# Performance work log

Measured on AMD Instinct MI355X. Metric: run time of the kernel, lower is better.

Reference implementation:

```python
import jax, jax.numpy as jnp
import numpy as np

MIN_SCORE = 0.3       # min_score_threshold
NMS_THRESHOLD = 0.3   # nms_threshold
MAX_OUT = 256         # fixed output padding (jit-compatible replacement for dynamic K)


def _cxcywh_to_xyxy(b):
    cx, cy, w, h = b[..., 0], b[..., 1], b[..., 2], b[..., 3]
    half_w, half_h = w * 0.5, h * 0.5
    return jnp.stack([cx - half_w, cy - half_h, cx + half_w, cy + half_h], axis=-1)


def _pairwise_iou(a, b):
    # a: [N,4], b: [M,4] in xyxy
    lt = jnp.maximum(a[:, None, :2], b[None, :, :2])
    rb = jnp.minimum(a[:, None, 2:], b[None, :, 2:])
    wh = jnp.clip(rb - lt, 0.0)
    inter = wh[..., 0] * wh[..., 1]
    area_a = (a[:, 2] - a[:, 0]) * (a[:, 3] - a[:, 1])
    area_b = (b[:, 2] - b[:, 0]) * (b[:, 3] - b[:, 1])
    return inter / (area_a[:, None] + area_b[None, :] - inter + 1e-9)


def setup_inputs() -> dict:
    key = jax.random.key(0)
    k1, k2 = jax.random.split(key)
    N, n_coords = 8192, 16
    score = jax.random.uniform(k1, (N, 1), dtype=jnp.float32)
    box = jax.random.uniform(k2, (N, n_coords), dtype=jnp.float32)
    return {"score": score, "box": box}


def reference(score, box):
    # score: [N,1], box: [N,n_coords]; single class (n_classes==1, cls=None)
    s = score[:, 0]
    valid = s >= MIN_SCORE                      # score mask applied before NMS
    order = jnp.argsort(-s)                     # score-descending (batched_nms order)
    s_s = s[order]
    v_s = valid[order]
    box_s = box[order]
    bbox = _cxcywh_to_xyxy(box_s[:, :4]).astype(jnp.float32)
    iou = _pairwise_iou(bbox, bbox)             # [N,N]
    N = s.shape[0]

    def body(kept, i):
        # suppressed if overlaps any already-kept (higher-score) box
        suppressed = jnp.any(kept & (iou[:, i] > NMS_THRESHOLD))
        keep_i = v_s[i] & jnp.logical_not(suppressed)
        return kept.at[i].set(keep_i), None

    kept, _ = jax.lax.scan(body, jnp.zeros((N,), dtype=bool), jnp.arange(N))

    # compact kept detections to the front, preserving score order (stable sort)
    comp = jnp.argsort(jnp.where(kept, 0, 1), stable=True)[:MAX_OUT]
    out_valid = kept[comp]                      # [MAX_OUT]
    score_out = jnp.where(out_valid[:, None], s_s[comp][:, None], 0.0)   # [MAX_OUT,1]
    box_out = jnp.where(out_valid[:, None], box_s[comp], 0.0)            # [MAX_OUT,n_coords]
    return score_out, box_out, out_valid
```

## Files before the change

### kernel.cpp

```cpp
#include <hip/hip_runtime.h>
#include <stdint.h>

typedef unsigned long long u64;

#define N 8192
#define NW 128
#define MAX_OUT 256
#define MASK_BYTES ((size_t)N * NW * 8)


__global__ __launch_bounds__(1024)
void rank_fused_kernel(const float* __restrict__ score, const float* __restrict__ box,
                       int* __restrict__ order, float* __restrict__ s_s,
                       float4* __restrict__ bbox, float* __restrict__ area,
                       int* __restrict__ nvalid) {
    __shared__ uint32_t ksc[N];
    __shared__ int psum[32][33];
    __shared__ int vpart[16];
    const int tid = threadIdx.x;

    const float4* s4 = (const float4*)score;
    float4 a = s4[tid * 2], b = s4[tid * 2 + 1];
    ksc[tid * 8 + 0] = __float_as_uint(a.x);
    ksc[tid * 8 + 1] = __float_as_uint(a.y);
    ksc[tid * 8 + 2] = __float_as_uint(a.z);
    ksc[tid * 8 + 3] = __float_as_uint(a.w);
    ksc[tid * 8 + 4] = __float_as_uint(b.x);
    ksc[tid * 8 + 5] = __float_as_uint(b.y);
    ksc[tid * 8 + 6] = __float_as_uint(b.z);
    ksc[tid * 8 + 7] = __float_as_uint(b.w);
    int c = (a.x >= 0.3f) + (a.y >= 0.3f) + (a.z >= 0.3f) + (a.w >= 0.3f)
          + (b.x >= 0.3f) + (b.y >= 0.3f) + (b.z >= 0.3f) + (b.w >= 0.3f);
    for (int off = 32; off; off >>= 1) c += __shfl_down(c, off);
    if ((tid & 63) == 0) vpart[tid >> 6] = c;
    __syncthreads();
    if (blockIdx.x == 0 && tid == 0) {
        int t = 0;
        #pragma unroll
        for (int w = 0; w < 16; ++w) t += vpart[w];
        *nvalid = t;
    }

    const int i_local = tid & 31;
    const int jg = tid >> 5;
    const int ibase = blockIdx.x * 32;
    const uint32_t si = ksc[ibase + i_local];
    const int i = ibase + i_local;
    int cnt = 0;
    const int j0 = jg * 256;
    #pragma unroll 8
    for (int t = 0; t < 256; ++t) {
        const int j = j0 + t;
        const uint32_t sj = ksc[j];
        cnt += (sj > si || (sj == si && j < i)) ? 1 : 0;
    }
    psum[i_local][jg] = cnt;
    __syncthreads();

    if (tid < 32) {
        int r = 0;
        #pragma unroll
        for (int k = 0; k < 32; ++k) r += psum[tid][k];
        const int ii = ibase + tid;
        order[r] = ii;
        s_s[r] = score[ii];
        float4 cb = ((const float4*)box)[ii * 4];
        float hw = cb.z * 0.5f, hh = cb.w * 0.5f;
        float x0 = cb.x - hw, y0 = cb.y - hh, x1 = cb.x + hw, y1 = cb.y + hh;
        bbox[r] = make_float4(x0, y0, x1, y1);
        area[r] = (x1 - x0) * (y1 - y0);
    }
}

__global__ __launch_bounds__(256)
void mask_kernel(const float4* __restrict__ bbox, const float* __restrict__ area,
                 const int* __restrict__ nvalid_p, u64* __restrict__ maskT) {
    const int w = blockIdx.x;
    if (w < (int)(blockIdx.y << 2)) return;
    const int nv = *nvalid_p;
    if ((int)(blockIdx.y * 256) >= nv) return;
    __shared__ float4 jb[64];
    __shared__ float  ja[64];
    if (threadIdx.x < 64) {
        jb[threadIdx.x] = bbox[w * 64 + threadIdx.x];
        ja[threadIdx.x] = area[w * 64 + threadIdx.x];
    }
    __syncthreads();
    const int i = blockIdx.y * 256 + threadIdx.x;
    if (i >= nv) return;
    if (w < (i >> 6)) return;
    float4 aa4 = bbox[i];
    float  aa = area[i];
    u64 bits = 0, fb = 0;
    #pragma unroll 8
    for (int jj = 0; jj < 64; ++jj) {
        float4 b = jb[jj];
        float lx = fmaxf(aa4.x, b.x), ly = fmaxf(aa4.y, b.y);
        float rx = fminf(aa4.z, b.z), ry = fminf(aa4.w, b.w);
        float ww = fmaxf(rx - lx, 0.0f), hh = fmaxf(ry - ly, 0.0f);
        float inter = ww * hh;
        float denom = ((aa + ja[jj]) - inter) + 1e-9f;
        float d = fmaf(-0.3f, denom, inter);
        bits |= ((u64)(d > 0.0f)) << jj;
        fb   |= ((u64)(fabsf(d) <= 1e-5f * denom)) << jj;
    }
    if (fb) {
        while (fb) {
            int jj = (int)__builtin_ctzll(fb); fb &= fb - 1;
            float4 b = jb[jj];
            float lx = fmaxf(aa4.x, b.x), ly = fmaxf(aa4.y, b.y);
            float rx = fminf(aa4.z, b.z), ry = fminf(aa4.w, b.w);
            float ww = fmaxf(rx - lx, 0.0f), hh = fmaxf(ry - ly, 0.0f);
            float inter = ww * hh;
            float denom = ((aa + ja[jj]) - inter) + 1e-9f;
            float iou = inter / denom;
            bits = (bits & ~(1ull << jj)) | (((u64)(iou > 0.3f)) << jj);
        }
    }
    maskT[(size_t)w * N + i] = bits;
}

struct Pipe { u64 col, s1, s2, g0, g1, g2, g3; };

__device__ __forceinline__ unsigned or_dpp32(unsigned v) {
    v |= (unsigned)__builtin_amdgcn_update_dpp(0, (int)v, 0x111, 0xf, 0xf, true);
    v |= (unsigned)__builtin_amdgcn_update_dpp(0, (int)v, 0x112, 0xf, 0xf, true);
    v |= (unsigned)__builtin_amdgcn_update_dpp(0, (int)v, 0x114, 0xf, 0xf, true);
    v |= (unsigned)__builtin_amdgcn_update_dpp(0, (int)v, 0x118, 0xf, 0xf, true);
    v |= (unsigned)__builtin_amdgcn_update_dpp(0, (int)v, 0x142, 0xf, 0xf, true);
    v |= (unsigned)__builtin_amdgcn_update_dpp(0, (int)v, 0x143, 0xf, 0xf, true);
    return v;
}

__device__ __forceinline__ u64 wave_or64(u64 v) {
    unsigned lo = or_dpp32((unsigned)v);
    unsigned hi = or_dpp32((unsigned)(v >> 32));
    unsigned slo = (unsigned)__builtin_amdgcn_readlane((int)lo, 63);
    unsigned shi = (unsigned)__builtin_amdgcn_readlane((int)hi, 63);
    return ((u64)shi << 32) | (u64)slo;
}

__global__ __launch_bounds__(64)
void nms_kernel(const u64* __restrict__ maskT, const float* __restrict__ s_s,
                const int* __restrict__ order, const float* __restrict__ box,
                const int* __restrict__ nvalid_p, float* __restrict__ out) {
    const int lane = threadIdx.x;
    const int nv = *nvalid_p;
    const int nblk = (nv + 63) >> 6;
    int kcount = 0;
    int kp0 = 0, kp1 = 0, kp2 = 0, kp3 = 0;
    u64 s1m = 0, s2m = 0, s2m_old = 0;

    Pipe A, B;
    A.col = A.s1 = A.s2 = A.g0 = A.g1 = A.g2 = A.g3 = 0;
    B.col = B.s1 = B.s2 = B.g0 = B.g1 = B.g2 = B.g3 = 0;
    if (nblk > 0) {
        A.col = maskT[lane];
        if (nblk > 1) A.s1 = maskT[(size_t)1 * N + lane];
        if (nblk > 2) A.s2 = maskT[(size_t)2 * N + lane];
    }
    if (nblk > 1) {
        B.col = maskT[(size_t)1 * N + 64 + lane];
        if (nblk > 2) B.s1 = maskT[(size_t)2 * N + 64 + lane];
        if (nblk > 3) B.s2 = maskT[(size_t)3 * N + 64 + lane];
    }

    auto step = [&](int b, Pipe& P) -> bool {
        u64 col = P.col, s1v = P.s1, s2v = P.s2;
        u64 x = P.g0 | P.g1 | P.g2 | P.g3 | s1m | s2m_old;
        const int b2 = b + 2;
        P.col = P.s1 = P.s2 = P.g0 = P.g1 = P.g2 = P.g3 = 0;
        if (b2 < nblk) {
            const int row = (b2 << 6) + lane;
            P.col = maskT[(size_t)b2 * N + row];
            if (b2 + 1 < nblk) P.s1 = maskT[(size_t)(b2 + 1) * N + row];
            if (b2 + 2 < nblk) P.s2 = maskT[(size_t)(b2 + 2) * N + row];
            const int kc = kcount;
            const u64* colw = maskT + (size_t)b2 * N;
            if (lane < kc)       P.g0 = colw[kp0];
            if (lane +  64 < kc) P.g1 = colw[kp1];
            if (lane + 128 < kc) P.g2 = colw[kp2];
            if (lane + 192 < kc) P.g3 = colw[kp3];
        }
        u64 rw = wave_or64(x);
        const int base = b << 6;
        const int rem = nv - base;
        u64 validm = (rem >= 64) ? ~0ull : ((1ull << rem) - 1ull);
        u64 todo = validm & ~rw;
        u64 km = 0;
        while (todo) {
            int l = (int)__builtin_ctzll(todo);
            u64 row_l = __ballot(((col >> l) & 1ull) != 0);
            const int pos = base + l;
            const bool own = (lane == (kcount & 63));
            const int slot = kcount >> 6;
            kp0 = (own && slot == 0) ? pos : kp0;
            kp1 = (own && slot == 1) ? pos : kp1;
            kp2 = (own && slot == 2) ? pos : kp2;
            kp3 = (own && slot == 3) ? pos : kp3;
            km |= (1ull << l);
            kcount++;
            todo &= ~(row_l | (1ull << l));
            if (kcount >= MAX_OUT) break;
        }
        u64 keepm = ((km >> lane) & 1ull) ? ~0ull : 0ull;
        s2m_old = s2m;
        s2m = s2v & keepm;
        s1m = s1v & keepm;
        return kcount < MAX_OUT;
    };

    bool run = true;
    for (int b = 0; run && b < nblk; b += 2) {
        run = step(b, A);
        if (run && b + 1 < nblk) run = step(b + 1, B);
    }

    float* out_score = out;
    float* out_box   = out + MAX_OUT;
    float* out_valid = out + MAX_OUT + MAX_OUT * 16;
    const float4* box4 = (const float4*)box;
    float4* ob4 = (float4*)out_box;
    #define EMIT_SLOT(Q, KP) do {                                              \
        const int t = lane + 64 * (Q);                                         \
        if (t < kcount) {                                                      \
            int p = (KP);                                                      \
            out_score[t] = s_s[p];                                             \
            out_valid[t] = 1.0f;                                               \
            int oi = order[p];                                                 \
            _Pragma("unroll")                                                  \
            for (int q = 0; q < 4; ++q) ob4[t * 4 + q] = box4[oi * 4 + q];     \
        } else {                                                               \
            out_score[t] = 0.0f;                                               \
            out_valid[t] = 0.0f;                                               \
            float4 z = make_float4(0.f, 0.f, 0.f, 0.f);                        \
            _Pragma("unroll")                                                  \
            for (int q = 0; q < 4; ++q) ob4[t * 4 + q] = z;                    \
        }                                                                      \
    } while (0)
    EMIT_SLOT(0, kp0);
    EMIT_SLOT(1, kp1);
    EMIT_SLOT(2, kp2);
    EMIT_SLOT(3, kp3);
    #undef EMIT_SLOT
}

extern "C" void kernel_launch(void* const* d_in, const int* in_sizes, int n_in,
                              void* d_out, int out_size, void* d_ws, size_t ws_size,
                              hipStream_t stream) {
    const float* score = (const float*)d_in[0];
    const float* box   = (const float*)d_in[1];
    char* ws = (char*)d_ws;
    u64*    maskT  = (u64*)ws;
    int*    order  = (int*)   (ws + MASK_BYTES);
    float*  s_s    = (float*) (ws + MASK_BYTES + 32768);
    float4* bbox   = (float4*)(ws + MASK_BYTES + 65536);
    float*  area   = (float*) (ws + MASK_BYTES + 65536 + 131072);
    int*    nvalid = (int*)   (ws + MASK_BYTES + 65536 + 131072 + 32768);

    rank_fused_kernel<<<256, 1024, 0, stream>>>(score, box, order, s_s, bbox, area, nvalid);
    mask_kernel<<<dim3(128, 32), 256, 0, stream>>>(bbox, area, nvalid, maskT);
    nms_kernel<<<1, 64, 0, stream>>>(maskT, s_s, order, box, nvalid, (float*)d_out);
}
```

Baseline: 128.1 us.

## Process NMS in 128-box superblocks with in-loop cross-block suppression

Restructures the serial NMS scan to handle two 64-box blocks per iteration. Suppression of the second block by boxes kept in the first is folded in during the first block's loop via readlane ORs, and carries from both blocks are merged for the next two word columns. This halves the number of wave-wide OR reductions and loop iterations on the serial critical path. The cost is an extra pair of readlanes per kept box, more registers, and more prefetch loads per iteration.

```diff
diff --git a/kernel.cpp b/kernel.cpp
--- a/kernel.cpp
+++ b/kernel.cpp
@@ -120,7 +120,6 @@
     maskT[(size_t)w * N + i] = bits;
 }
 
-struct Pipe { u64 col, s1, s2, g0, g1, g2, g3; };
 
 __device__ __forceinline__ unsigned or_dpp32(unsigned v) {
     v |= (unsigned)__builtin_amdgcn_update_dpp(0, (int)v, 0x111, 0xf, 0xf, true);
@@ -140,6 +139,9 @@
     return ((u64)shi << 32) | (u64)slo;
 }
 
+#define RL64(v, l) ( ((u64)(unsigned)__builtin_amdgcn_readlane((int)(unsigned)((v) >> 32), (l)) << 32) \
+                   |  (u64)(unsigned)__builtin_amdgcn_readlane((int)(unsigned)(v), (l)) )
+
 __global__ __launch_bounds__(64)
 void nms_kernel(const u64* __restrict__ maskT, const float* __restrict__ s_s,
                 const int* __restrict__ order, const float* __restrict__ box,
@@ -147,50 +149,87 @@
     const int lane = threadIdx.x;
     const int nv = *nvalid_p;
     const int nblk = (nv + 63) >> 6;
+    const int nst = (nblk + 1) >> 1;
     int kcount = 0;
     int kp0 = 0, kp1 = 0, kp2 = 0, kp3 = 0;
-    u64 s1m = 0, s2m = 0, s2m_old = 0;
-
-    Pipe A, B;
-    A.col = A.s1 = A.s2 = A.g0 = A.g1 = A.g2 = A.g3 = 0;
-    B.col = B.s1 = B.s2 = B.g0 = B.g1 = B.g2 = B.g3 = 0;
-    if (nblk > 0) {
-        A.col = maskT[lane];
-        if (nblk > 1) A.s1 = maskT[(size_t)1 * N + lane];
-        if (nblk > 2) A.s2 = maskT[(size_t)2 * N + lane];
-    }
-    if (nblk > 1) {
-        B.col = maskT[(size_t)1 * N + 64 + lane];
-        if (nblk > 2) B.s1 = maskT[(size_t)2 * N + 64 + lane];
-        if (nblk > 3) B.s2 = maskT[(size_t)3 * N + 64 + lane];
-    }
-
-    auto step = [&](int b, Pipe& P) -> bool {
-        u64 col = P.col, s1v = P.s1, s2v = P.s2;
-        u64 x = P.g0 | P.g1 | P.g2 | P.g3 | s1m | s2m_old;
-        const int b2 = b + 2;
-        P.col = P.s1 = P.s2 = P.g0 = P.g1 = P.g2 = P.g3 = 0;
-        if (b2 < nblk) {
-            const int row = (b2 << 6) + lane;
-            P.col = maskT[(size_t)b2 * N + row];
-            if (b2 + 1 < nblk) P.s1 = maskT[(size_t)(b2 + 1) * N + row];
-            if (b2 + 2 < nblk) P.s2 = maskT[(size_t)(b2 + 2) * N + row];
+    u64 carry0 = 0, carry1 = 0;
+
+    u64 pc00 = 0, pc10 = 0, pc11 = 0;
+    u64 ps00 = 0, ps01 = 0, ps10 = 0, ps11 = 0;
+    u64 pg0=0, pg1=0, pg2=0, pg3=0, ph0=0, ph1=0, ph2=0, ph3=0;
+
+    if (nst > 0) {
+        pc00 = maskT[lane];
+        if (1 < nblk) {
+            pc10 = maskT[(size_t)1 * N + lane];
+            pc11 = maskT[(size_t)1 * N + 64 + lane];
+        }
+        if (2 < nblk) {
+            ps00 = maskT[(size_t)2 * N + lane];
+            ps01 = maskT[(size_t)2 * N + 64 + lane];
+        }
+        if (3 < nblk) {
+            ps10 = maskT[(size_t)3 * N + lane];
+            ps11 = maskT[(size_t)3 * N + 64 + lane];
+        }
+    }
+
+    for (int t = 0; t < nst && kcount < MAX_OUT; ++t) {
+        u64 c00 = pc00, c10 = pc10, c11 = pc11;
+        u64 x0 = pg0 | pg1 | pg2 | pg3 | carry0;
+        u64 x1 = ph0 | ph1 | ph2 | ph3 | carry1;
+        u64 s00 = ps00, s01 = ps01, s10 = ps10, s11 = ps11;
+
+        pc00 = pc10 = pc11 = 0;
+        ps00 = ps01 = ps10 = ps11 = 0;
+        pg0 = pg1 = pg2 = pg3 = ph0 = ph1 = ph2 = ph3 = 0;
+        const int t1 = t + 1;
+        if (t1 < nst) {
+            const int w0n = t1 << 1, w1n = w0n | 1;
+            const size_t r0n = ((size_t)t1 << 7) + lane;
+            const u64* cw0 = maskT + (size_t)w0n * N;
             const int kc = kcount;
-            const u64* colw = maskT + (size_t)b2 * N;
-            if (lane < kc)       P.g0 = colw[kp0];
-            if (lane +  64 < kc) P.g1 = colw[kp1];
-            if (lane + 128 < kc) P.g2 = colw[kp2];
-            if (lane + 192 < kc) P.g3 = colw[kp3];
-        }
-        u64 rw = wave_or64(x);
-        const int base = b << 6;
-        const int rem = nv - base;
-        u64 validm = (rem >= 64) ? ~0ull : ((1ull << rem) - 1ull);
-        u64 todo = validm & ~rw;
-        u64 km = 0;
+            pc00 = cw0[r0n];
+            if (lane < kc)        pg0 = cw0[kp0];
+            if (lane +  64 < kc)  pg1 = cw0[kp1];
+            if (lane + 128 < kc)  pg2 = cw0[kp2];
+            if (lane + 192 < kc)  pg3 = cw0[kp3];
+            if (w1n < nblk) {
+                const u64* cw1 = maskT + (size_t)w1n * N;
+                pc10 = cw1[r0n];
+                pc11 = cw1[r0n + 64];
+                if (lane < kc)        ph0 = cw1[kp0];
+                if (lane +  64 < kc)  ph1 = cw1[kp1];
+                if (lane + 128 < kc)  ph2 = cw1[kp2];
+                if (lane + 192 < kc)  ph3 = cw1[kp3];
+            }
+            const int ws0 = w0n + 2, ws1 = w0n + 3;
+            if (ws0 < nblk) {
+                const u64* sw0 = maskT + (size_t)ws0 * N;
+                ps00 = sw0[r0n];
+                ps01 = sw0[r0n + 64];
+            }
+            if (ws1 < nblk) {
+                const u64* sw1 = maskT + (size_t)ws1 * N;
+                ps10 = sw1[r0n];
+                ps11 = sw1[r0n + 64];
+            }
+        }
+
+        u64 rw0 = wave_or64(x0);
+        u64 rw1 = wave_or64(x1);
+
+        const int base = t << 7;
+        const int rem0 = nv - base;
+        const int rem1 = rem0 - 64;
+        u64 vm0 = (rem0 >= 64) ? ~0ull : ((1ull << rem0) - 1ull);
+        u64 vm1 = (rem1 >= 64) ? ~0ull : ((rem1 > 0) ? ((1ull << rem1) - 1ull) : 0ull);
+
+        u64 km0 = 0, km1 = 0;
+        u64 todo = vm0 & ~rw0;
         while (todo) {
             int l = (int)__builtin_ctzll(todo);
-            u64 row_l = __ballot(((col >> l) & 1ull) != 0);
+            u64 row_l = __ballot(((c00 >> l) & 1ull) != 0);
             const int pos = base + l;
             const bool own = (lane == (kcount & 63));
             const int slot = kcount >> 6;
@@ -198,22 +237,34 @@
             kp1 = (own && slot == 1) ? pos : kp1;
             kp2 = (own && slot == 2) ? pos : kp2;
             kp3 = (own && slot == 3) ? pos : kp3;
-            km |= (1ull << l);
+            km0 |= 1ull << l;
             kcount++;
             todo &= ~(row_l | (1ull << l));
+            rw1 |= RL64(c10, l);
             if (kcount >= MAX_OUT) break;
         }
-        u64 keepm = ((km >> lane) & 1ull) ? ~0ull : 0ull;
-        s2m_old = s2m;
-        s2m = s2v & keepm;
-        s1m = s1v & keepm;
-        return kcount < MAX_OUT;
-    };
-
-    bool run = true;
-    for (int b = 0; run && b < nblk; b += 2) {
-        run = step(b, A);
-        if (run && b + 1 < nblk) run = step(b + 1, B);
+        if (kcount < MAX_OUT) {
+            todo = vm1 & ~rw1;
+            while (todo) {
+                int l = (int)__builtin_ctzll(todo);
+                u64 row_l = __ballot(((c11 >> l) & 1ull) != 0);
+                const int pos = base + 64 + l;
+                const bool own = (lane == (kcount & 63));
+                const int slot = kcount >> 6;
+                kp0 = (own && slot == 0) ? pos : kp0;
+                kp1 = (own && slot == 1) ? pos : kp1;
+                kp2 = (own && slot == 2) ? pos : kp2;
+                kp3 = (own && slot == 3) ? pos : kp3;
+                km1 |= 1ull << l;
+                kcount++;
+                todo &= ~(row_l | (1ull << l));
+                if (kcount >= MAX_OUT) break;
+            }
+        }
+        u64 keepm0 = ((km0 >> lane) & 1ull) ? ~0ull : 0ull;
+        u64 keepm1 = ((km1 >> lane) & 1ull) ? ~0ull : 0ull;
+        carry0 = (s00 & keepm0) | (s01 & keepm1);
+        carry1 = (s10 & keepm0) | (s11 & keepm1);
     }
 
     float* out_score = out;
```

New measurement: 129.9 us. No clear change (+1.4%).

## Process NMS blocks in 128-row super-steps with dual-word prefetch pipeline

Applied to the files above, without the earlier changes.

Restructures the serial NMS sweep so each pipeline stage handles two 64-bit mask words (128 boxes) at once. The kept-list gather loads, carries and prefetches are issued for both words together, and suppression from the first half feeds the second half via readlane. The aim is to halve the number of serial stage transitions and wave-wide OR reductions, so more memory latency hides behind the dependent ballot loop. The cost is many more live 64-bit registers and extra prefetched loads, some of which may be wasted after early termination.

```diff
diff --git a/kernel.cpp b/kernel.cpp
--- a/kernel.cpp
+++ b/kernel.cpp
@@ -120,7 +120,6 @@
     maskT[(size_t)w * N + i] = bits;
 }
 
-struct Pipe { u64 col, s1, s2, g0, g1, g2, g3; };
 
 __device__ __forceinline__ unsigned or_dpp32(unsigned v) {
     v |= (unsigned)__builtin_amdgcn_update_dpp(0, (int)v, 0x111, 0xf, 0xf, true);
@@ -140,80 +139,151 @@
     return ((u64)shi << 32) | (u64)slo;
 }
 
-__global__ __launch_bounds__(64)
+#define RL64(v, l) ( ((u64)(unsigned)__builtin_amdgcn_readlane((int)(unsigned)((v) >> 32), (l)) << 32) \
+                   |  (u64)(unsigned)__builtin_amdgcn_readlane((int)(unsigned)(v), (l)) )
+
+#define NMS_STEP(T, PC00,PC10,PC11, S1A0,S1A1,S1B0,S1B1, S2A0,S2A1,S2B0,S2B1,  \
+                 G0,G1,G2,G3, H0,H1,H2,H3) do {                                \
+    const int t_ = (T);                                                        \
+                   \
+    u64 c00_ = PC00, c10_ = PC10, c11_ = PC11;                                 \
+    u64 x0_ = G0 | G1 | G2 | G3 | carry1_0 | carry2_0;                         \
+    u64 x1_ = H0 | H1 | H2 | H3 | carry1_1 | carry2_1;                         \
+    u64 s1a0_=S1A0, s1a1_=S1A1, s1b0_=S1B0, s1b1_=S1B1;                        \
+    u64 s2a0_=S2A0, s2a1_=S2A1, s2b0_=S2B0, s2b1_=S2B1;                        \
+         \
+    PC00=0; PC10=0; PC11=0;                                                    \
+    S1A0=0; S1A1=0; S1B0=0; S1B1=0; S2A0=0; S2A1=0; S2B0=0; S2B1=0;            \
+    G0=0; G1=0; G2=0; G3=0; H0=0; H1=0; H2=0; H3=0;                            \
+    const int t2_ = t_ + 2;                                                    \
+    if (t2_ < nst) {                                                           \
+        const int w0n_ = t2_ << 1, w1n_ = w0n_ | 1;                            \
+        const size_t r0_ = ((size_t)t2_ << 7) + lane;                          \
+        const u64* cw0_ = maskT + (size_t)w0n_ * N;                            \
+        const int kc_ = kcount;                                                \
+        PC00 = cw0_[r0_];                                                      \
+        if (lane < kc_)        G0 = cw0_[kp0];                                 \
+        if (lane +  64 < kc_)  G1 = cw0_[kp1];                                 \
+        if (lane + 128 < kc_)  G2 = cw0_[kp2];                                 \
+        if (lane + 192 < kc_)  G3 = cw0_[kp3];                                 \
+        if (w1n_ < nblk) {                                                     \
+            const u64* cw1_ = maskT + (size_t)w1n_ * N;                        \
+            PC10 = cw1_[r0_];                                                  \
+            PC11 = cw1_[r0_ + 64];                                             \
+            if (lane < kc_)        H0 = cw1_[kp0];                             \
+            if (lane +  64 < kc_)  H1 = cw1_[kp1];                             \
+            if (lane + 128 < kc_)  H2 = cw1_[kp2];                             \
+            if (lane + 192 < kc_)  H3 = cw1_[kp3];                             \
+        }                                                                      \
+        if (w0n_ + 2 < nblk) { const u64* p_ = maskT + (size_t)(w0n_+2)*N;     \
+                               S1A0 = p_[r0_]; S1A1 = p_[r0_ + 64]; }          \
+        if (w0n_ + 3 < nblk) { const u64* p_ = maskT + (size_t)(w0n_+3)*N;     \
+                               S1B0 = p_[r0_]; S1B1 = p_[r0_ + 64]; }          \
+        if (w0n_ + 4 < nblk) { const u64* p_ = maskT + (size_t)(w0n_+4)*N;     \
+                               S2A0 = p_[r0_]; S2A1 = p_[r0_ + 64]; }          \
+        if (w0n_ + 5 < nblk) { const u64* p_ = maskT + (size_t)(w0n_+5)*N;     \
+                               S2B0 = p_[r0_]; S2B1 = p_[r0_ + 64]; }          \
+    }                                                                          \
+                           \
+    u64 rw0_ = wave_or64(x0_);                                                 \
+    u64 rw1_ = wave_or64(x1_);                                                 \
+    const int base_ = t_ << 7;                                                 \
+    const int rem0_ = nv - base_;                                              \
+    const int rem1_ = rem0_ - 64;                                              \
+    u64 vm0_ = (rem0_ >= 64) ? ~0ull : ((1ull << rem0_) - 1ull);               \
+    u64 vm1_ = (rem1_ >= 64) ? ~0ull : ((rem1_ > 0) ? ((1ull << rem1_) - 1ull) : 0ull); \
+    u64 km0_ = 0, km1_ = 0;                                                    \
+    u64 todo_ = vm0_ & ~rw0_;                                                  \
+    while (todo_) {                                                            \
+        int l_ = (int)__builtin_ctzll(todo_);                                  \
+        u64 rowl_ = __ballot(((c00_ >> l_) & 1ull) != 0);                      \
+        const int pos_ = base_ + l_;                                           \
+        const bool own_ = (lane == (kcount & 63));                             \
+        const int slot_ = kcount >> 6;                                         \
+        kp0 = (own_ && slot_ == 0) ? pos_ : kp0;                               \
+        kp1 = (own_ && slot_ == 1) ? pos_ : kp1;                               \
+        kp2 = (own_ && slot_ == 2) ? pos_ : kp2;                               \
+        kp3 = (own_ && slot_ == 3) ? pos_ : kp3;                               \
+        km0_ |= 1ull << l_;                                                    \
+        kcount++;                                                              \
+        todo_ &= ~(rowl_ | (1ull << l_));                                      \
+        rw1_ |= RL64(c10_, l_);                                                \
+        if (kcount >= MAX_OUT) break;                                          \
+    }                                                                          \
+    if (kcount < MAX_OUT) {                                                    \
+        todo_ = vm1_ & ~rw1_;                                                  \
+        while (todo_) {                                                        \
+            int l_ = (int)__builtin_ctzll(todo_);                              \
+            u64 rowl_ = __ballot(((c11_ >> l_) & 1ull) != 0);                  \
+            const int pos_ = base_ + 64 + l_;                                  \
+            const bool own_ = (lane == (kcount & 63));                         \
+            const int slot_ = kcount >> 6;                                     \
+            kp0 = (own_ && slot_ == 0) ? pos_ : kp0;                           \
+            kp1 = (own_ && slot_ == 1) ? pos_ : kp1;                           \
+            kp2 = (own_ && slot_ == 2) ? pos_ : kp2;                           \
+            kp3 = (own_ && slot_ == 3) ? pos_ : kp3;                           \
+            km1_ |= 1ull << l_;                                                \
+            kcount++;                                                          \
+            todo_ &= ~(rowl_ | (1ull << l_));                                  \
+            if (kcount >= MAX_OUT) break;                                      \
+        }                                                                      \
+    }                                                                          \
+          \
+    u64 keepm0_ = ((km0_ >> lane) & 1ull) ? ~0ull : 0ull;                      \
+    u64 keepm1_ = ((km1_ >> lane) & 1ull) ? ~0ull : 0ull;                      \
+    carry1_0 = (s1a0_ & keepm0_) | (s1a1_ & keepm1_);                          \
+    carry1_1 = (s1b0_ & keepm0_) | (s1b1_ & keepm1_);                          \
+    carry2_0 = c2pend0; carry2_1 = c2pend1;                                    \
+    c2pend0 = (s2a0_ & keepm0_) | (s2a1_ & keepm1_);                           \
+    c2pend1 = (s2b0_ & keepm0_) | (s2b1_ & keepm1_);                           \
+} while (0)
+
+__global__ __launch_bounds__(64, 1)
 void nms_kernel(const u64* __restrict__ maskT, const float* __restrict__ s_s,
                 const int* __restrict__ order, const float* __restrict__ box,
                 const int* __restrict__ nvalid_p, float* __restrict__ out) {
     const int lane = threadIdx.x;
     const int nv = *nvalid_p;
     const int nblk = (nv + 63) >> 6;
+    const int nst = (nblk + 1) >> 1;
     int kcount = 0;
     int kp0 = 0, kp1 = 0, kp2 = 0, kp3 = 0;
-    u64 s1m = 0, s2m = 0, s2m_old = 0;
-
-    Pipe A, B;
-    A.col = A.s1 = A.s2 = A.g0 = A.g1 = A.g2 = A.g3 = 0;
-    B.col = B.s1 = B.s2 = B.g0 = B.g1 = B.g2 = B.g3 = 0;
-    if (nblk > 0) {
-        A.col = maskT[lane];
-        if (nblk > 1) A.s1 = maskT[(size_t)1 * N + lane];
-        if (nblk > 2) A.s2 = maskT[(size_t)2 * N + lane];
-    }
-    if (nblk > 1) {
-        B.col = maskT[(size_t)1 * N + 64 + lane];
-        if (nblk > 2) B.s1 = maskT[(size_t)2 * N + 64 + lane];
-        if (nblk > 3) B.s2 = maskT[(size_t)3 * N + 64 + lane];
-    }
-
-    auto step = [&](int b, Pipe& P) -> bool {
-        u64 col = P.col, s1v = P.s1, s2v = P.s2;
-        u64 x = P.g0 | P.g1 | P.g2 | P.g3 | s1m | s2m_old;
-        const int b2 = b + 2;
-        P.col = P.s1 = P.s2 = P.g0 = P.g1 = P.g2 = P.g3 = 0;
-        if (b2 < nblk) {
-            const int row = (b2 << 6) + lane;
-            P.col = maskT[(size_t)b2 * N + row];
-            if (b2 + 1 < nblk) P.s1 = maskT[(size_t)(b2 + 1) * N + row];
-            if (b2 + 2 < nblk) P.s2 = maskT[(size_t)(b2 + 2) * N + row];
-            const int kc = kcount;
-            const u64* colw = maskT + (size_t)b2 * N;
-            if (lane < kc)       P.g0 = colw[kp0];
-            if (lane +  64 < kc) P.g1 = colw[kp1];
-            if (lane + 128 < kc) P.g2 = colw[kp2];
-            if (lane + 192 < kc) P.g3 = colw[kp3];
-        }
-        u64 rw = wave_or64(x);
-        const int base = b << 6;
-        const int rem = nv - base;
-        u64 validm = (rem >= 64) ? ~0ull : ((1ull << rem) - 1ull);
-        u64 todo = validm & ~rw;
-        u64 km = 0;
-        while (todo) {
-            int l = (int)__builtin_ctzll(todo);
-            u64 row_l = __ballot(((col >> l) & 1ull) != 0);
-            const int pos = base + l;
-            const bool own = (lane == (kcount & 63));
-            const int slot = kcount >> 6;
-            kp0 = (own && slot == 0) ? pos : kp0;
-            kp1 = (own && slot == 1) ? pos : kp1;
-            kp2 = (own && slot == 2) ? pos : kp2;
-            kp3 = (own && slot == 3) ? pos : kp3;
-            km |= (1ull << l);
-            kcount++;
-            todo &= ~(row_l | (1ull << l));
-            if (kcount >= MAX_OUT) break;
-        }
-        u64 keepm = ((km >> lane) & 1ull) ? ~0ull : 0ull;
-        s2m_old = s2m;
-        s2m = s2v & keepm;
-        s1m = s1v & keepm;
-        return kcount < MAX_OUT;
-    };
-
-    bool run = true;
-    for (int b = 0; run && b < nblk; b += 2) {
-        run = step(b, A);
-        if (run && b + 1 < nblk) run = step(b + 1, B);
+    u64 carry1_0 = 0, carry1_1 = 0;
+    u64 carry2_0 = 0, carry2_1 = 0;
+    u64 c2pend0 = 0, c2pend1 = 0;
+
+    u64 apc00=0, apc10=0, apc11=0;
+    u64 as1a0=0, as1a1=0, as1b0=0, as1b1=0, as2a0=0, as2a1=0, as2b0=0, as2b1=0;
+    u64 ag0=0, ag1=0, ag2=0, ag3=0, ah0=0, ah1=0, ah2=0, ah3=0;
+    u64 bpc00=0, bpc10=0, bpc11=0;
+    u64 bs1a0=0, bs1a1=0, bs1b0=0, bs1b1=0, bs2a0=0, bs2a1=0, bs2b0=0, bs2b1=0;
+    u64 bg0=0, bg1=0, bg2=0, bg3=0, bh0=0, bh1=0, bh2=0, bh3=0;
+
+    if (nst > 0) {
+        const size_t r0 = (size_t)lane;
+        apc00 = maskT[r0];
+        if (1 < nblk) { apc10 = maskT[(size_t)1*N + r0]; apc11 = maskT[(size_t)1*N + r0 + 64]; }
+        if (2 < nblk) { as1a0 = maskT[(size_t)2*N + r0]; as1a1 = maskT[(size_t)2*N + r0 + 64]; }
+        if (3 < nblk) { as1b0 = maskT[(size_t)3*N + r0]; as1b1 = maskT[(size_t)3*N + r0 + 64]; }
+        if (4 < nblk) { as2a0 = maskT[(size_t)4*N + r0]; as2a1 = maskT[(size_t)4*N + r0 + 64]; }
+        if (5 < nblk) { as2b0 = maskT[(size_t)5*N + r0]; as2b1 = maskT[(size_t)5*N + r0 + 64]; }
+    }
+    if (1 < nst) {
+        const size_t r1 = (size_t)128 + lane;
+        bpc00 = maskT[(size_t)2*N + r1];
+        if (3 < nblk) { bpc10 = maskT[(size_t)3*N + r1]; bpc11 = maskT[(size_t)3*N + r1 + 64]; }
+        if (4 < nblk) { bs1a0 = maskT[(size_t)4*N + r1]; bs1a1 = maskT[(size_t)4*N + r1 + 64]; }
+        if (5 < nblk) { bs1b0 = maskT[(size_t)5*N + r1]; bs1b1 = maskT[(size_t)5*N + r1 + 64]; }
+        if (6 < nblk) { bs2a0 = maskT[(size_t)6*N + r1]; bs2a1 = maskT[(size_t)6*N + r1 + 64]; }
+        if (7 < nblk) { bs2b0 = maskT[(size_t)7*N + r1]; bs2b1 = maskT[(size_t)7*N + r1 + 64]; }
+    }
+
+    for (int t = 0; t < nst && kcount < MAX_OUT; t += 2) {
+        NMS_STEP(t, apc00,apc10,apc11, as1a0,as1a1,as1b0,as1b1,
+                 as2a0,as2a1,as2b0,as2b1, ag0,ag1,ag2,ag3, ah0,ah1,ah2,ah3);
+        if (t + 1 < nst && kcount < MAX_OUT)
+            NMS_STEP(t + 1, bpc00,bpc10,bpc11, bs1a0,bs1a1,bs1b0,bs1b1,
+                     bs2a0,bs2a1,bs2b0,bs2b1, bg0,bg1,bg2,bg3, bh0,bh1,bh2,bh3);
     }
 
     float* out_score = out;
```

Result: slower. 131.1 us (+2.3%).

## Track removal bitmask per lane via row loads instead of gathered columns

Applied to the files above, without the earlier changes.

Replaces the per-block gather of kept boxes' column words plus a wave-wide DPP OR reduction with a running per-lane removal vector (two u64 words covering 128 blocks). Each lane accumulates the mask rows of newly kept boxes, and the block's suppression word is read with readlane. Immediate next-block suppression is handled by readlane of the s1 row for each kept box, and the first four kept rows are prefetched and deferred one step. This aims to shorten the serial dependency chain per block, at the cost of strided per-lane loads and extra readlane loops proportional to kept boxes.

```diff
diff --git a/kernel.cpp b/kernel.cpp
--- a/kernel.cpp
+++ b/kernel.cpp
@@ -120,27 +120,84 @@
     maskT[(size_t)w * N + i] = bits;
 }
 
-struct Pipe { u64 col, s1, s2, g0, g1, g2, g3; };
-
-__device__ __forceinline__ unsigned or_dpp32(unsigned v) {
-    v |= (unsigned)__builtin_amdgcn_update_dpp(0, (int)v, 0x111, 0xf, 0xf, true);
-    v |= (unsigned)__builtin_amdgcn_update_dpp(0, (int)v, 0x112, 0xf, 0xf, true);
-    v |= (unsigned)__builtin_amdgcn_update_dpp(0, (int)v, 0x114, 0xf, 0xf, true);
-    v |= (unsigned)__builtin_amdgcn_update_dpp(0, (int)v, 0x118, 0xf, 0xf, true);
-    v |= (unsigned)__builtin_amdgcn_update_dpp(0, (int)v, 0x142, 0xf, 0xf, true);
-    v |= (unsigned)__builtin_amdgcn_update_dpp(0, (int)v, 0x143, 0xf, 0xf, true);
-    return v;
-}
-
-__device__ __forceinline__ u64 wave_or64(u64 v) {
-    unsigned lo = or_dpp32((unsigned)v);
-    unsigned hi = or_dpp32((unsigned)(v >> 32));
-    unsigned slo = (unsigned)__builtin_amdgcn_readlane((int)lo, 63);
-    unsigned shi = (unsigned)__builtin_amdgcn_readlane((int)hi, 63);
-    return ((u64)shi << 32) | (u64)slo;
-}
-
-__global__ __launch_bounds__(64)
+
+#define RL64(v, l) ( ((u64)(unsigned)__builtin_amdgcn_readlane((int)(unsigned)((v) >> 32), (l)) << 32) \
+                   |  (u64)(unsigned)__builtin_amdgcn_readlane((int)(unsigned)(v), (l)) )
+
+#define NMS_STEP(B, PCOL, PS1, D0,D1,D2,D3,D4,D5,D6,D7, DCNT) do {            \
+    const int b_ = (B);                                                        \
+      \
+    {                                                                          \
+        const int c_ = DCNT;                                                   \
+        remv0 |= (c_ > 0 ? D0 : 0) | (c_ > 1 ? D2 : 0)                         \
+               | (c_ > 2 ? D4 : 0) | (c_ > 3 ? D6 : 0);                        \
+        remv1 |= (c_ > 0 ? D1 : 0) | (c_ > 1 ? D3 : 0)                         \
+               | (c_ > 2 ? D5 : 0) | (c_ > 3 ? D7 : 0);                        \
+    }                                                                          \
+                                  \
+    u64 sel_ = (b_ < 64) ? remv0 : remv1;                                      \
+    u64 rw_ = RL64(sel_, b_ & 63) | rsup;                                      \
+                 \
+    u64 col_ = PCOL;                                                           \
+    u64 s1v_ = (b_ + 1 < nblk) ? PS1 : 0;                                      \
+           \
+    {                                                                          \
+        const int nb1_ = nblk - 1;                                             \
+        const int bc_ = (b_ + 2 < nb1_) ? (b_ + 2) : nb1_;                     \
+        const int w1_ = (b_ + 3 < nb1_) ? (b_ + 3) : nb1_;                     \
+        const int row_ = (bc_ << 6) + lane;                                    \
+        PCOL = maskT[(size_t)bc_ * N + row_];                                  \
+        PS1  = maskT[(size_t)w1_ * N + row_];                                  \
+    }                                                                          \
+                                                               \
+    const int base_ = b_ << 6;                                                 \
+    const int rem_ = nv - base_;                                               \
+    u64 validm_ = (rem_ >= 64) ? ~0ull : ((1ull << rem_) - 1ull);              \
+    u64 todo_ = validm_ & ~rw_;                                                \
+    u64 km_ = 0;                                                               \
+    while (todo_) {                                                            \
+        int l_ = (int)__builtin_ctzll(todo_);                                  \
+        u64 rowl_ = __ballot(((col_ >> l_) & 1ull) != 0);                      \
+        const int pos_ = base_ + l_;                                           \
+        const bool own_ = (lane == (kcount & 63));                             \
+        const int slot_ = kcount >> 6;                                         \
+        kp0 = (own_ && slot_ == 0) ? pos_ : kp0;                               \
+        kp1 = (own_ && slot_ == 1) ? pos_ : kp1;                               \
+        kp2 = (own_ && slot_ == 2) ? pos_ : kp2;                               \
+        kp3 = (own_ && slot_ == 3) ? pos_ : kp3;                               \
+        km_ |= (1ull << l_);                                                   \
+        kcount++;                                                              \
+           \
+        todo_ &= ~(rowl_ | (1ull << l_));                                      \
+        if (kcount >= MAX_OUT) break;                                          \
+    }                                                                          \
+    \
+    u64 add1_ = 0, t_ = km_;                                                   \
+    while (t_) { int l_ = (int)__builtin_ctzll(t_); t_ &= t_ - 1;              \
+                 add1_ |= RL64(s1v_, l_); }                                    \
+    rsup = add1_;                                                              \
+        \
+    {                                                                          \
+        u64 t2_ = km_;                                                         \
+        int r0_ = base_, r1_ = base_, r2_ = base_, r3_ = base_, c2_ = 0;       \
+        if (t2_) { r0_ = base_ + (int)__builtin_ctzll(t2_); t2_ &= t2_ - 1; c2_ = 1; } \
+        if (t2_) { r1_ = base_ + (int)__builtin_ctzll(t2_); t2_ &= t2_ - 1; c2_ = 2; } \
+        if (t2_) { r2_ = base_ + (int)__builtin_ctzll(t2_); t2_ &= t2_ - 1; c2_ = 3; } \
+        if (t2_) { r3_ = base_ + (int)__builtin_ctzll(t2_); t2_ &= t2_ - 1; c2_ = 4; } \
+        D0 = maskT[woffL + r0_]; D1 = maskT[woffH + r0_];                      \
+        D2 = maskT[woffL + r1_]; D3 = maskT[woffH + r1_];                      \
+        D4 = maskT[woffL + r2_]; D5 = maskT[woffH + r2_];                      \
+        D6 = maskT[woffL + r3_]; D7 = maskT[woffH + r3_];                      \
+        DCNT = c2_;                                                            \
+                \
+        while (t2_) { int l_ = (int)__builtin_ctzll(t2_); t2_ &= t2_ - 1;      \
+                      const int r_ = base_ + l_;                               \
+                      remv0 |= maskT[woffL + r_]; remv1 |= maskT[woffH + r_]; }\
+    }                                                                          \
+    run = (kcount < MAX_OUT);                                                  \
+} while (0)
+
+__global__ __launch_bounds__(64, 1)
 void nms_kernel(const u64* __restrict__ maskT, const float* __restrict__ s_s,
                 const int* __restrict__ order, const float* __restrict__ box,
                 const int* __restrict__ nvalid_p, float* __restrict__ out) {
@@ -149,71 +206,32 @@
     const int nblk = (nv + 63) >> 6;
     int kcount = 0;
     int kp0 = 0, kp1 = 0, kp2 = 0, kp3 = 0;
-    u64 s1m = 0, s2m = 0, s2m_old = 0;
-
-    Pipe A, B;
-    A.col = A.s1 = A.s2 = A.g0 = A.g1 = A.g2 = A.g3 = 0;
-    B.col = B.s1 = B.s2 = B.g0 = B.g1 = B.g2 = B.g3 = 0;
+    u64 remv0 = 0, remv1 = 0, rsup = 0;
+    const size_t woffL = (size_t)lane * N;
+    const size_t woffH = (size_t)(64 + lane) * N;
+
+    u64 Acol = 0, As1 = 0, Bcol = 0, Bs1 = 0;
+    u64 da0=0,da1=0,da2=0,da3=0,da4=0,da5=0,da6=0,da7=0; int dcntA = 0;
+    u64 db0=0,db1=0,db2=0,db3=0,db4=0,db5=0,db6=0,db7=0; int dcntB = 0;
+
     if (nblk > 0) {
-        A.col = maskT[lane];
-        if (nblk > 1) A.s1 = maskT[(size_t)1 * N + lane];
-        if (nblk > 2) A.s2 = maskT[(size_t)2 * N + lane];
-    }
-    if (nblk > 1) {
-        B.col = maskT[(size_t)1 * N + 64 + lane];
-        if (nblk > 2) B.s1 = maskT[(size_t)2 * N + 64 + lane];
-        if (nblk > 3) B.s2 = maskT[(size_t)3 * N + 64 + lane];
-    }
-
-    auto step = [&](int b, Pipe& P) -> bool {
-        u64 col = P.col, s1v = P.s1, s2v = P.s2;
-        u64 x = P.g0 | P.g1 | P.g2 | P.g3 | s1m | s2m_old;
-        const int b2 = b + 2;
-        P.col = P.s1 = P.s2 = P.g0 = P.g1 = P.g2 = P.g3 = 0;
-        if (b2 < nblk) {
-            const int row = (b2 << 6) + lane;
-            P.col = maskT[(size_t)b2 * N + row];
-            if (b2 + 1 < nblk) P.s1 = maskT[(size_t)(b2 + 1) * N + row];
-            if (b2 + 2 < nblk) P.s2 = maskT[(size_t)(b2 + 2) * N + row];
-            const int kc = kcount;
-            const u64* colw = maskT + (size_t)b2 * N;
-            if (lane < kc)       P.g0 = colw[kp0];
-            if (lane +  64 < kc) P.g1 = colw[kp1];
-            if (lane + 128 < kc) P.g2 = colw[kp2];
-            if (lane + 192 < kc) P.g3 = colw[kp3];
+        const int nb1 = nblk - 1;
+        const int w1 = (1 < nb1) ? 1 : nb1;
+        Acol = maskT[lane];
+        As1  = maskT[(size_t)w1 * N + lane];
+        if (nblk > 1) {
+            const int w2 = (2 < nb1) ? 2 : nb1;
+            const int row = 64 + lane;
+            Bcol = maskT[(size_t)1 * N + row];
+            Bs1  = maskT[(size_t)w2 * N + row];
         }
-        u64 rw = wave_or64(x);
-        const int base = b << 6;
-        const int rem = nv - base;
-        u64 validm = (rem >= 64) ? ~0ull : ((1ull << rem) - 1ull);
-        u64 todo = validm & ~rw;
-        u64 km = 0;
-        while (todo) {
-            int l = (int)__builtin_ctzll(todo);
-            u64 row_l = __ballot(((col >> l) & 1ull) != 0);
-            const int pos = base + l;
-            const bool own = (lane == (kcount & 63));
-            const int slot = kcount >> 6;
-            kp0 = (own && slot == 0) ? pos : kp0;
-            kp1 = (own && slot == 1) ? pos : kp1;
-            kp2 = (own && slot == 2) ? pos : kp2;
-            kp3 = (own && slot == 3) ? pos : kp3;
-            km |= (1ull << l);
-            kcount++;
-            todo &= ~(row_l | (1ull << l));
-            if (kcount >= MAX_OUT) break;
-        }
-        u64 keepm = ((km >> lane) & 1ull) ? ~0ull : 0ull;
-        s2m_old = s2m;
-        s2m = s2v & keepm;
-        s1m = s1v & keepm;
-        return kcount < MAX_OUT;
-    };
+    }
 
     bool run = true;
     for (int b = 0; run && b < nblk; b += 2) {
-        run = step(b, A);
-        if (run && b + 1 < nblk) run = step(b + 1, B);
+        NMS_STEP(b, Acol, As1, da0,da1,da2,da3,da4,da5,da6,da7, dcntA);
+        if (run && b + 1 < nblk)
+            NMS_STEP(b + 1, Bcol, Bs1, db0,db1,db2,db3,db4,db5,db6,db7, dcntB);
     }
 
     float* out_score = out;
```

New measurement: 178.8 us. 1.4x slower.
